# Performance work log

Hardware: AMD Instinct MI355X
Metric: run time of the kernel (lower is better)

Reference implementation:

```python
import jax, jax.numpy as jnp
import numpy as np

N = 50000
E = 800000
DIN = 128
HID = 128
H = 4
C = HID // H  # 32
NEG_SLOPE = 0.2


def _lin(k, fin, fout):
    return jax.random.normal(k, (fin, fout), jnp.float32) * (1.0 / np.sqrt(fin))


def setup_inputs() -> dict:
    key = jax.random.key(0)
    ks = jax.random.split(key, 24)
    x = jax.random.normal(ks[0], (N, DIN), jnp.float32)
    src = jax.random.randint(ks[1], (E,), 0, N)
    dst = (src + jax.random.randint(ks[2], (E,), 1, N)) % N  # no self-loops
    edge_index = jnp.stack([src, dst]).astype(jnp.int32)
    edge_weight = jax.random.uniform(ks[3], (E,), jnp.float32)
    p = {}
    for i, koff in ((0, 4), (1, 12)):
        fin = DIN if i == 0 else HID
        p[f"Wl{i}"] = _lin(ks[koff + 0], fin, HID)
        p[f"bl{i}"] = jnp.zeros((HID,), jnp.float32)
        p[f"Wr{i}"] = _lin(ks[koff + 1], fin, HID)
        p[f"br{i}"] = jnp.zeros((HID,), jnp.float32)
        p[f"We{i}"] = _lin(ks[koff + 2], 1, HID)
        p[f"att{i}"] = jax.random.normal(ks[koff + 3], (H, C), jnp.float32) * (1.0 / np.sqrt(C))
        p[f"b{i}"] = jnp.zeros((HID,), jnp.float32)
    p["prelu_a"] = jnp.float32(0.25)
    return dict(x=x, edge_index=edge_index, edge_weight=edge_weight, **p)


def gatv2_layer(x, src, dst, ea, Wl, bl, Wr, br, We, att, bias):
    n = x.shape[0]
    # self-loop edge_attr = per-dst mean of incoming edge_attr (fill_value='mean')
    deg = jax.ops.segment_sum(jnp.ones((ea.shape[0],), ea.dtype), dst, num_segments=n)
    loop_ea = jax.ops.segment_sum(ea, dst, num_segments=n) / jnp.maximum(deg, 1.0)[:, None]
    loops = jnp.arange(n, dtype=src.dtype)
    srcf = jnp.concatenate([src, loops])
    dstf = jnp.concatenate([dst, loops])
    eaf = jnp.concatenate([ea, loop_ea], axis=0)
    xl = (x @ Wl + bl).reshape(n, H, C)  # source transform (lin_l)
    xr = (x @ Wr + br).reshape(n, H, C)  # target transform (lin_r)
    eproj = (eaf @ We).reshape(-1, H, C)  # lin_edge, bias=False
    m = xl[srcf] + xr[dstf] + eproj  # [E+N, H, C]
    s = jnp.where(m >= 0, m, NEG_SLOPE * m)  # LeakyReLU(0.2)
    logits = jnp.einsum("ehc,hc->eh", s, att)
    # segment softmax over dst
    lmax = jax.lax.stop_gradient(jax.ops.segment_max(logits, dstf, num_segments=n))
    a = jnp.exp(logits - lmax[dstf])
    denom = jax.ops.segment_sum(a, dstf, num_segments=n)
    a = a / denom[dstf]
    out = jax.ops.segment_sum(a[:, :, None] * xl[srcf], dstf, num_segments=n)
    return out.reshape(n, H * C) + bias


def reference(x, edge_index, edge_weight,
              Wl0, bl0, Wr0, br0, We0, att0, b0,
              Wl1, bl1, Wr1, br1, We1, att1, b1,
              prelu_a):
    src, dst = edge_index[0], edge_index[1]
    ea = edge_weight[:, None]  # [E, 1]
    h = gatv2_layer(x, src, dst, ea, Wl0, bl0, Wr0, br0, We0, att0, b0)
    h = jnp.where(h >= 0, h, prelu_a * h)  # PReLU (dropout=0 -> identity)
    h = gatv2_layer(h, src, dst, ea, Wl1, bl1, Wr1, br1, We1, att1, b1)
    return h
```

## Files before the change

### kernel.cpp

```cpp
#include <hip/hip_runtime.h>
#include <hip/hip_bf16.h>
#include <math.h>

#define NN 50000
#define NE 800000
#define HD 128
#define MNEG (-1e30f)
#define LOG2E 1.44269504088896340736f

typedef __attribute__((ext_vector_type(8))) short short8;
typedef __attribute__((ext_vector_type(16))) float f32x16;

__global__ void k_edge_count(const int* __restrict__ ei,
                             int* __restrict__ deg, int* __restrict__ rank) {
    int e = blockIdx.x * blockDim.x + threadIdx.x;
    if (e >= NE) return;
    int d = ei[NE + e];
    rank[e] = atomicAdd(&deg[d], 1);
}

__global__ void k_scan1(const int* __restrict__ deg, int* __restrict__ offs,
                        int* __restrict__ bsums) {
    __shared__ int sh[256];
    int t = threadIdx.x;
    int i = blockIdx.x * 256 + t;
    int v = (i < NN) ? deg[i] : 0;
    sh[t] = v;
    __syncthreads();
    for (int off = 1; off < 256; off <<= 1) {
        int x = (t >= off) ? sh[t - off] : 0;
        __syncthreads();
        sh[t] += x;
        __syncthreads();
    }
    if (i < NN) offs[i] = sh[t] - v;
    if (t == 255) bsums[blockIdx.x] = sh[255];
}

__global__ void k_scan2(int* __restrict__ bsums, int nb) {
    __shared__ int sh[256];
    int t = threadIdx.x;
    int v = (t < nb) ? bsums[t] : 0;
    sh[t] = v;
    __syncthreads();
    for (int off = 1; off < 256; off <<= 1) {
        int x = (t >= off) ? sh[t - off] : 0;
        __syncthreads();
        sh[t] += x;
        __syncthreads();
    }
    if (t < nb) bsums[t] = sh[t] - v;
}

__global__ void k_scan3(int* __restrict__ offs, const int* __restrict__ bsums) {
    int i = blockIdx.x * 256 + threadIdx.x;
    if (i == 0) offs[NN] = NE;
    if (i >= NN) return;
    offs[i] += bsums[blockIdx.x];
}

__global__ void k_csr_fill(const int* __restrict__ ei, const float* __restrict__ ew,
                           const int* __restrict__ rank, const int* __restrict__ offs,
                           int2* __restrict__ csr) {
    int e = blockIdx.x * blockDim.x + threadIdx.x;
    if (e >= NE) return;
    int d = ei[NE + e];
    csr[offs[d] + rank[e]] = make_int2(ei[e], __float_as_int(ew[e]));
}

__device__ __forceinline__ void f2bf2(float x, short& h, short& l) {
    __hip_bfloat16 hb = __float2bfloat16(x);
    float hf = __bfloat162float(hb);
    __hip_bfloat16 lb = __float2bfloat16(x - hf);
    h = *reinterpret_cast<short*>(&hb);
    l = *reinterpret_cast<short*>(&lb);
}

__device__ __forceinline__ void load8(const float* __restrict__ p, float* r) {
    float4 t0 = *(const float4*)p;
    float4 t1 = *(const float4*)(p + 4);
    r[0] = t0.x; r[1] = t0.y; r[2] = t0.z; r[3] = t0.w;
    r[4] = t1.x; r[5] = t1.y; r[6] = t1.z; r[7] = t1.w;
}

__global__ void k_pack(const float* __restrict__ Wl, const float* __restrict__ Wr,
                       short* __restrict__ bhi, short* __restrict__ blo) {
    int idx = blockIdx.x * blockDim.x + threadIdx.x;
    if (idx >= 8 * 8 * 64 * 8) return;
    int j = idx & 7;
    int lane = (idx >> 3) & 63;
    int q = (idx >> 9) & 7;
    int t = idx >> 12;
    int col = t * 32 + (lane & 31);
    int k = q * 16 + ((lane >> 5) << 3) + j;
    float v = (col < 128) ? Wl[k * 128 + col] : Wr[k * 128 + (col - 128)];
    short h, l;
    f2bf2(v, h, l);
    bhi[idx] = h;
    blo[idx] = l;
}

template <bool AF32>
__global__ __launch_bounds__(256, 2) void k_gemm_mfma(
        const float* __restrict__ Af,
        const short* __restrict__ Ahi, const short* __restrict__ Alo,
        const short* __restrict__ Bhi, const short* __restrict__ Blo,
        const float* __restrict__ bl, const float* __restrict__ br,
        float* __restrict__ outl, float* __restrict__ outr) {
    int wave = blockIdx.x * 4 + (threadIdx.x >> 6);
    int lane = threadIdx.x & 63;
    int m0 = wave * 32;
    if (m0 >= NN) return;

    int arow = m0 + (lane & 31);
    size_t abase = (size_t)(arow < NN ? arow : 0) * HD + ((lane >> 5) << 3);

    f32x16 acc[8];
#pragma unroll
    for (int t = 0; t < 8; ++t)
#pragma unroll
        for (int r = 0; r < 16; ++r) acc[t][r] = 0.f;

    const short8* Bh8 = (const short8*)Bhi;
    const short8* Bl8 = (const short8*)Blo;

#pragma unroll
    for (int q = 0; q < 8; ++q) {
        short8 ah, al;
        if constexpr (AF32) {
            float vv[8];
            load8(&Af[abase + q * 16], vv);
#pragma unroll
            for (int k2 = 0; k2 < 8; ++k2) {
                short h, l;
                f2bf2(vv[k2], h, l);
                ah[k2] = h;
                al[k2] = l;
            }
        } else {
            ah = *(const short8*)(Ahi + abase + q * 16);
            al = *(const short8*)(Alo + abase + q * 16);
        }
#pragma unroll
        for (int t = 0; t < 8; ++t) {
            short8 bh = Bh8[(t * 8 + q) * 64 + lane];
            short8 bl_ = Bl8[(t * 8 + q) * 64 + lane];
            acc[t] = __builtin_amdgcn_mfma_f32_32x32x16_bf16(ah, bh, acc[t], 0, 0, 0);
            acc[t] = __builtin_amdgcn_mfma_f32_32x32x16_bf16(al, bh, acc[t], 0, 0, 0);
            acc[t] = __builtin_amdgcn_mfma_f32_32x32x16_bf16(ah, bl_, acc[t], 0, 0, 0);
        }
    }

    int colr = lane & 31;
    int rowoff = (lane >> 5) << 2;
#pragma unroll
    for (int t = 0; t < 8; ++t) {
        int colg = t * 32 + colr;
        float bias = (colg < 128) ? bl[colg] : br[colg - 128];
        float* dst = (colg < 128) ? (outl + colg) : (outr + (colg - 128));
#pragma unroll
        for (int r = 0; r < 16; ++r) {
            int rw = m0 + (r & 3) + ((r >> 2) << 3) + rowoff;
            if (rw < NN) dst[(size_t)rw * HD] = acc[t][r] + bias;
        }
    }
}


__device__ __forceinline__ float dotpart(const float* xv, const float* xrv,
                                         const float* wev, const float* atv, float w) {
    float part = 0.f;
#pragma unroll
    for (int k = 0; k < 8; ++k) {
        float t = fmaf(w, wev[k], xrv[k]) + xv[k];
        t = fmaxf(t, 0.2f * t);
        part = fmaf(atv[k], t, part);
    }
    part += __shfl_xor(part, 1);
    part += __shfl_xor(part, 2);
    return part;
}

__device__ __forceinline__ void upd(float part, const float* xv,
                                    float& m, float& s, float* o) {
    bool nm = part > m + 11.5f;
    if (__any(nm)) {
        float newm = nm ? part : m;
        float sc = exp2f(m - newm);
        s *= sc;
#pragma unroll
        for (int k = 0; k < 8; ++k) o[k] *= sc;
        m = newm;
    }
    float p = exp2f(part - m);
    s += p;
#pragma unroll
    for (int k = 0; k < 8; ++k) o[k] = fmaf(p, xv[k], o[k]);
}

template <bool PRELU, bool OUTBF>
__global__ __launch_bounds__(256) void k_node(
        const float* __restrict__ xl, const float* __restrict__ xr,
        const int* __restrict__ offs, const int2* __restrict__ csr,
        const float* __restrict__ We, const float* __restrict__ att,
        const float* __restrict__ bias, const float* __restrict__ prelu,
        float* __restrict__ out, short* __restrict__ ohi, short* __restrict__ olo) {
    int wid = (blockIdx.x * blockDim.x + threadIdx.x) >> 6;
    if (wid >= NN) return;
    const int lane = threadIdx.x & 63;
    const int g = lane >> 4;
    const int j = lane & 15;
    const int c0 = j << 3;
    const int v = wid;

    float xrv[8], wev[8], atv[8];
    load8(&xr[(size_t)v * HD + c0], xrv);
    load8(&We[c0], wev);
    load8(&att[c0], atv);
#pragma unroll
    for (int k = 0; k < 8; ++k) atv[k] *= LOG2E;

    const int beg = offs[v];
    const int deg = offs[v + 1] - beg;

    float m = MNEG, s = 0.f, wsum = 0.f;
    float o[8];
#pragma unroll
    for (int k = 0; k < 8; ++k) o[k] = 0.f;

    int i = g;
    for (; i + 4 < deg; i += 8) {
        int2 e0 = csr[beg + i];
        int2 e1 = csr[beg + i + 4];
        float w0 = __int_as_float(e0.y), w1 = __int_as_float(e1.y);
        float xv0[8], xv1[8];
        load8(&xl[(size_t)e0.x * HD + c0], xv0);
        load8(&xl[(size_t)e1.x * HD + c0], xv1);
        float p0 = dotpart(xv0, xrv, wev, atv, w0);
        float p1 = dotpart(xv1, xrv, wev, atv, w1);
        upd(p0, xv0, m, s, o);
        upd(p1, xv1, m, s, o);
        wsum += w0 + w1;
    }
    if (i < deg) {
        int2 e0 = csr[beg + i];
        float w0 = __int_as_float(e0.y);
        float xv0[8];
        load8(&xl[(size_t)e0.x * HD + c0], xv0);
        float p0 = dotpart(xv0, xrv, wev, atv, w0);
        upd(p0, xv0, m, s, o);
        wsum += w0;
    }

#pragma unroll
    for (int d = 16; d < 64; d <<= 1) {
        float m2 = __shfl_xor(m, d);
        float s2 = __shfl_xor(s, d);
        wsum += __shfl_xor(wsum, d);
        float M = fmaxf(m, m2);
        float a = exp2f(m - M), b = exp2f(m2 - M);
        s = s * a + s2 * b;
#pragma unroll
        for (int k = 0; k < 8; ++k) {
            float o2 = __shfl_xor(o[k], d);
            o[k] = o[k] * a + o2 * b;
        }
        m = M;
    }

    {
        float wself = wsum / fmaxf((float)deg, 1.f);
        float xv[8];
        load8(&xl[(size_t)v * HD + c0], xv);
        float part = dotpart(xv, xrv, wev, atv, wself);
        float newm = fmaxf(m, part);
        float a = exp2f(m - newm), p = exp2f(part - newm);
        s = s * a + p;
#pragma unroll
        for (int k = 0; k < 8; ++k) o[k] = fmaf(o[k], a, p * xv[k]);
    }

    if (g == 0) {
        float bi[8];
        load8(&bias[c0], bi);
        float inv = 1.f / s;
        float r[8];
#pragma unroll
        for (int k = 0; k < 8; ++k) r[k] = fmaf(o[k], inv, bi[k]);
        if (PRELU) {
            float a = *prelu;
#pragma unroll
            for (int k = 0; k < 8; ++k) r[k] = (r[k] >= 0.f) ? r[k] : a * r[k];
        }
        if (OUTBF) {
            short8 h8, l8;
#pragma unroll
            for (int k = 0; k < 8; ++k) {
                short h, l;
                f2bf2(r[k], h, l);
                h8[k] = h;
                l8[k] = l;
            }
            *(short8*)&ohi[(size_t)v * HD + c0] = h8;
            *(short8*)&olo[(size_t)v * HD + c0] = l8;
        } else {
            float* op = &out[(size_t)v * HD + c0];
            *(float4*)op = make_float4(r[0], r[1], r[2], r[3]);
            *(float4*)(op + 4) = make_float4(r[4], r[5], r[6], r[7]);
        }
    }
}

extern "C" void kernel_launch(void* const* d_in, const int* in_sizes, int n_in,
                              void* d_out, int out_size, void* d_ws, size_t ws_size,
                              hipStream_t stream) {
    const float* x    = (const float*)d_in[0];
    const int*   ei   = (const int*)d_in[1];
    const float* ew   = (const float*)d_in[2];
    const float* Wl0  = (const float*)d_in[3];
    const float* bl0  = (const float*)d_in[4];
    const float* Wr0  = (const float*)d_in[5];
    const float* br0  = (const float*)d_in[6];
    const float* We0  = (const float*)d_in[7];
    const float* att0 = (const float*)d_in[8];
    const float* b0   = (const float*)d_in[9];
    const float* Wl1  = (const float*)d_in[10];
    const float* bl1  = (const float*)d_in[11];
    const float* Wr1  = (const float*)d_in[12];
    const float* br1  = (const float*)d_in[13];
    const float* We1  = (const float*)d_in[14];
    const float* att1 = (const float*)d_in[15];
    const float* b1   = (const float*)d_in[16];
    const float* prelu= (const float*)d_in[17];
    float* out = (float*)d_out;

    char* ws = (char*)d_ws;
    size_t off = 0;
    auto alloc = [&](size_t bytes) {
        char* p = ws + off;
        off += (bytes + 255) & ~size_t(255);
        return p;
    };
    float* bufA   = (float*)alloc(sizeof(float) * NN * HD);
    float* bufB   = (float*)alloc(sizeof(float) * NN * HD);
    short* ahi    = (short*)alloc(sizeof(short) * NN * HD);
    short* alo    = (short*)alloc(sizeof(short) * NN * HD);
    int*   deg    = (int*)alloc(sizeof(int) * NN);
    int*   rank   = (int*)alloc(sizeof(int) * NE);
    int*   offs   = (int*)alloc(sizeof(int) * (NN + 1));
    int*   bsums  = (int*)alloc(sizeof(int) * 256);
    int2*  csr    = (int2*)alloc(sizeof(int2) * NE);
    short* bp0h   = (short*)alloc(sizeof(short) * 32768);
    short* bp0l   = (short*)alloc(sizeof(short) * 32768);
    short* bp1h   = (short*)alloc(sizeof(short) * 32768);
    short* bp1l   = (short*)alloc(sizeof(short) * 32768);
    (void)ws_size; (void)in_sizes; (void)n_in; (void)out_size;

    hipMemsetAsync(deg, 0, sizeof(int) * NN, stream);

    const int EB = (NE + 255) / 256;
    const int NB = (NN + 255) / 256;

    k_edge_count<<<EB, 256, 0, stream>>>(ei, deg, rank);
    k_scan1<<<NB, 256, 0, stream>>>(deg, offs, bsums);
    k_scan2<<<1, 256, 0, stream>>>(bsums, NB);
    k_scan3<<<NB, 256, 0, stream>>>(offs, bsums);
    k_csr_fill<<<EB, 256, 0, stream>>>(ei, ew, rank, offs, csr);

    k_pack<<<128, 256, 0, stream>>>(Wl0, Wr0, bp0h, bp0l);
    k_pack<<<128, 256, 0, stream>>>(Wl1, Wr1, bp1h, bp1l);

    const int GB = (NN + 127) / 128;
    const int VB = (NN * 64 + 255) / 256;

    k_gemm_mfma<true><<<GB, 256, 0, stream>>>(x, nullptr, nullptr, bp0h, bp0l,
                                              bl0, br0, bufA, bufB);
    k_node<true, true><<<VB, 256, 0, stream>>>(bufA, bufB, offs, csr,
                                               We0, att0, b0, prelu,
                                               nullptr, ahi, alo);
    k_gemm_mfma<false><<<GB, 256, 0, stream>>>(nullptr, ahi, alo, bp1h, bp1l,
                                               bl1, br1, bufA, bufB);
    k_node<false, false><<<VB, 256, 0, stream>>>(bufA, bufB, offs, csr,
                                                 We1, att1, b1, nullptr,
                                                 out, nullptr, nullptr);
}
```

Baseline: 413.5 us.

## Split GEMM output columns across blocks and use dual-accumulator branchless online softmax

The GEMM kernel now gives each block only half of the 256 output columns: the grid doubles and each wave holds 4 accumulator tiles instead of 8. This cuts register pressure so the launch bound can allow 3 blocks per CU, at the cost of loading or converting each A row twice. In the node kernel, the online softmax update no longer uses the lazy wave-wide __any rescale check and always rescales. Two independent accumulator sets take alternating edges to break the serial dependency chain, and they are merged before the cross-group reduction.

```diff
diff --git a/kernel.cpp b/kernel.cpp
--- a/kernel.cpp
+++ b/kernel.cpp
@@ -101,23 +101,24 @@
 }
 
 template <bool AF32>
-__global__ __launch_bounds__(256, 2) void k_gemm_mfma(
+__global__ __launch_bounds__(256, 3) void k_gemm_mfma(
         const float* __restrict__ Af,
         const short* __restrict__ Ahi, const short* __restrict__ Alo,
         const short* __restrict__ Bhi, const short* __restrict__ Blo,
         const float* __restrict__ bl, const float* __restrict__ br,
         float* __restrict__ outl, float* __restrict__ outr) {
-    int wave = blockIdx.x * 4 + (threadIdx.x >> 6);
+    int ch = blockIdx.x & 1;
+    int rowblk = blockIdx.x >> 1;
     int lane = threadIdx.x & 63;
-    int m0 = wave * 32;
+    int m0 = rowblk * 128 + (threadIdx.x >> 6) * 32;
     if (m0 >= NN) return;
 
     int arow = m0 + (lane & 31);
     size_t abase = (size_t)(arow < NN ? arow : 0) * HD + ((lane >> 5) << 3);
 
-    f32x16 acc[8];
-#pragma unroll
-    for (int t = 0; t < 8; ++t)
+    f32x16 acc[4];
+#pragma unroll
+    for (int t = 0; t < 4; ++t)
 #pragma unroll
         for (int r = 0; r < 16; ++r) acc[t][r] = 0.f;
 
@@ -142,26 +143,27 @@
             al = *(const short8*)(Alo + abase + q * 16);
         }
 #pragma unroll
-        for (int t = 0; t < 8; ++t) {
+        for (int t2 = 0; t2 < 4; ++t2) {
+            int t = ch * 4 + t2;
             short8 bh = Bh8[(t * 8 + q) * 64 + lane];
             short8 bl_ = Bl8[(t * 8 + q) * 64 + lane];
-            acc[t] = __builtin_amdgcn_mfma_f32_32x32x16_bf16(ah, bh, acc[t], 0, 0, 0);
-            acc[t] = __builtin_amdgcn_mfma_f32_32x32x16_bf16(al, bh, acc[t], 0, 0, 0);
-            acc[t] = __builtin_amdgcn_mfma_f32_32x32x16_bf16(ah, bl_, acc[t], 0, 0, 0);
+            acc[t2] = __builtin_amdgcn_mfma_f32_32x32x16_bf16(ah, bh, acc[t2], 0, 0, 0);
+            acc[t2] = __builtin_amdgcn_mfma_f32_32x32x16_bf16(al, bh, acc[t2], 0, 0, 0);
+            acc[t2] = __builtin_amdgcn_mfma_f32_32x32x16_bf16(ah, bl_, acc[t2], 0, 0, 0);
         }
     }
 
     int colr = lane & 31;
     int rowoff = (lane >> 5) << 2;
 #pragma unroll
-    for (int t = 0; t < 8; ++t) {
-        int colg = t * 32 + colr;
+    for (int t2 = 0; t2 < 4; ++t2) {
+        int colg = (ch * 4 + t2) * 32 + colr;
         float bias = (colg < 128) ? bl[colg] : br[colg - 128];
         float* dst = (colg < 128) ? (outl + colg) : (outr + (colg - 128));
 #pragma unroll
         for (int r = 0; r < 16; ++r) {
             int rw = m0 + (r & 3) + ((r >> 2) << 3) + rowoff;
-            if (rw < NN) dst[(size_t)rw * HD] = acc[t][r] + bias;
+            if (rw < NN) dst[(size_t)rw * HD] = acc[t2][r] + bias;
         }
     }
 }
@@ -183,19 +185,13 @@
 
 __device__ __forceinline__ void upd(float part, const float* xv,
                                     float& m, float& s, float* o) {
-    bool nm = part > m + 11.5f;
-    if (__any(nm)) {
-        float newm = nm ? part : m;
-        float sc = exp2f(m - newm);
-        s *= sc;
-#pragma unroll
-        for (int k = 0; k < 8; ++k) o[k] *= sc;
-        m = newm;
-    }
-    float p = exp2f(part - m);
-    s += p;
-#pragma unroll
-    for (int k = 0; k < 8; ++k) o[k] = fmaf(p, xv[k], o[k]);
+    float newm = fmaxf(m, part);
+    float sc = exp2f(m - newm);
+    float p = exp2f(part - newm);
+    s = fmaf(s, sc, p);
+#pragma unroll
+    for (int k = 0; k < 8; ++k) o[k] = fmaf(o[k], sc, p * xv[k]);
+    m = newm;
 }
 
 template <bool PRELU, bool OUTBF>
@@ -223,10 +219,10 @@
     const int beg = offs[v];
     const int deg = offs[v + 1] - beg;
 
-    float m = MNEG, s = 0.f, wsum = 0.f;
-    float o[8];
-#pragma unroll
-    for (int k = 0; k < 8; ++k) o[k] = 0.f;
+    float mA = MNEG, sA = 0.f, mB = MNEG, sB = 0.f, wsum = 0.f;
+    float oA[8], oB[8];
+#pragma unroll
+    for (int k = 0; k < 8; ++k) { oA[k] = 0.f; oB[k] = 0.f; }
 
     int i = g;
     for (; i + 4 < deg; i += 8) {
@@ -238,8 +234,8 @@
         load8(&xl[(size_t)e1.x * HD + c0], xv1);
         float p0 = dotpart(xv0, xrv, wev, atv, w0);
         float p1 = dotpart(xv1, xrv, wev, atv, w1);
-        upd(p0, xv0, m, s, o);
-        upd(p1, xv1, m, s, o);
+        upd(p0, xv0, mA, sA, oA);
+        upd(p1, xv1, mB, sB, oB);
         wsum += w0 + w1;
     }
     if (i < deg) {
@@ -248,8 +244,17 @@
         float xv0[8];
         load8(&xl[(size_t)e0.x * HD + c0], xv0);
         float p0 = dotpart(xv0, xrv, wev, atv, w0);
-        upd(p0, xv0, m, s, o);
+        upd(p0, xv0, mA, sA, oA);
         wsum += w0;
+    }
+
+    float m, s, o[8];
+    {
+        m = fmaxf(mA, mB);
+        float a = exp2f(mA - m), b = exp2f(mB - m);
+        s = sA * a + sB * b;
+#pragma unroll
+        for (int k = 0; k < 8; ++k) o[k] = oA[k] * a + oB[k] * b;
     }
 
 #pragma unroll
@@ -370,7 +375,7 @@
     k_pack<<<128, 256, 0, stream>>>(Wl0, Wr0, bp0h, bp0l);
     k_pack<<<128, 256, 0, stream>>>(Wl1, Wr1, bp1h, bp1l);
 
-    const int GB = (NN + 127) / 128;
+    const int GB = 2 * ((NN + 127) / 128);
     const int VB = (NN * 64 + 255) / 256;
 
     k_gemm_mfma<true><<<GB, 256, 0, stream>>>(x, nullptr, nullptr, bp0h, bp0l,
```

Measured after the change: 367.8 us. 11.1% less time.
